# Kernel optimization log

Measured on AMD Instinct MI355X. Metric: run time of the kernel, lower is better.

## Reference

```python
import jax, jax.numpy as jnp
import numpy as np

B = 4096


def setup_inputs() -> dict:
    key = jax.random.key(0)
    u = jax.random.uniform(key, (B, 5), dtype=jnp.float32)
    centers = u[:, :2] * 64.0          # box centers in [0, 64)
    wh = u[:, 2:4] * 8.0 + 1.0         # widths/heights in [1, 9)
    ang = u[:, 4:5] * 3.14159265       # rotation angle in [0, pi)
    boxes = jnp.concatenate([centers, wh, ang], axis=-1)  # (B,5)
    return {"boxes": boxes}


def _rect_to_corners(boxes):
    # boxes: (B,5) = (x, y, w, h, theta) -> corners (B,4,2)
    unit = jnp.array([[-1.0, -1.0], [1.0, -1.0], [1.0, 1.0], [-1.0, 1.0]],
                     dtype=boxes.dtype)
    ctr, wh, ang = boxes[:, :2], boxes[:, 2:4], boxes[:, 4]
    base = unit[None, :, :] * (wh * 0.5)[:, None, :]        # (B,4,2)
    c, s = jnp.cos(ang), jnp.sin(ang)
    rot = jnp.stack([jnp.stack([c, -s], -1),
                     jnp.stack([s, c], -1)], axis=1)         # (B,2,2)
    return jnp.einsum('bkd,bde->bke', base, rot) + ctr[:, None, :]


def _giou1d(min1, max1, min2, max2):
    # exact (non-fast) 1-D GIoU per axis
    inter = jnp.clip(jnp.minimum(max1, max2) - jnp.maximum(min1, min2), 0.0)
    union = (max1 - min1) + (max2 - min2) - inter
    hull = jnp.maximum(max1, max2) - jnp.minimum(min1, min2)
    return inter / union - (hull - union) / hull


def reference(boxes):
    corners = _rect_to_corners(boxes)                        # (B,4,2)
    nb = corners.shape[0]
    # two edge axes per box: c1-c0 and c3-c0
    axes = jnp.stack([corners[:, 1] - corners[:, 0],
                      corners[:, 3] - corners[:, 0]], axis=1)  # (B,2,2)
    # self projections: box b's corners onto its own axes
    sp = jnp.einsum('bkd,bad->bak', corners, axes)           # (B,2,4)
    smin, smax = sp.min(-1), sp.max(-1)                      # (B,2)
    # cross projections: corners of box i onto axes of box j
    cp = jnp.einsum('ikd,jad->ijak', corners, axes)          # (B,B,2,4)
    cmin, cmax = cp.min(-1), cp.max(-1)                      # (B,B,2)
    # projections of box j's corners onto box i's axes = transpose of cross
    cminT, cmaxT = jnp.swapaxes(cmin, 0, 1), jnp.swapaxes(cmax, 0, 1)
    # axes of box i: (box i self) vs (box j projected on i's axes)
    gA = _giou1d(smin[:, None, :], smax[:, None, :], cminT, cmaxT)  # (B,B,2)
    # axes of box j: (box i projected on j's axes) vs (box j self)
    gB = _giou1d(cmin, cmax, smin[None, :, :], smax[None, :, :])    # (B,B,2)
    g = jnp.concatenate([gA, gB], axis=-1).min(-1)           # min over 4 axes
    pairwise = jnp.clip(g, 0.0)
    idx = jnp.arange(nb)
    pairwise = pairwise.at[idx, idx].set(0.0)                # zero diagonal
    return pairwise  # reduction='none' -> (B,B)
```

## Files before the change

### kernel.cpp

```cpp
#include <hip/hip_runtime.h>
#include <math.h>

#define NBOX 4096
#define TILE 32
#define NT (NBOX / TILE)
#define NTRI (NT * (NT + 1) / 2)
#define NBLK (NTRI / 4)
#define SS 12
#define JB 400
#define SLICE 800

typedef float v2f __attribute__((ext_vector_type(2)));
typedef float vf4 __attribute__((ext_vector_type(4)));


struct Box {
    v2f A0, A1, SC, LL;
    float cx, cy;
};

__device__ __forceinline__ float rcp_fast(float x) { return __builtin_amdgcn_rcpf(x); }
__device__ __forceinline__ v2f splat(float s) { return (v2f){s, s}; }
__device__ __forceinline__ v2f fma2(v2f a, v2f b, v2f c) { return __builtin_elementwise_fma(a, b, c); }
__device__ __forceinline__ v2f abs2(v2f a) { return __builtin_elementwise_abs(a); }
__device__ __forceinline__ v2f min2(v2f a, v2f b) { return __builtin_elementwise_min(a, b); }

__device__ __forceinline__ float mgiou_pair(const Box& I, const Box& J) {
    v2f dA = fma2(I.A0, splat(J.A0.x), I.A1 * J.A1.x);
    v2f dB = fma2(I.A0, splat(J.A0.y), I.A1 * J.A1.y);
    v2f DI = fma2(I.A0, splat(J.cx), fma2(I.A1, splat(J.cy), -I.SC));
    v2f DJ = fma2(J.A0, splat(I.cx), fma2(J.A1, splat(I.cy), -J.SC));
    v2f aA = abs2(dA), aB = abs2(dB);
    v2f HI = aA + aB;
    v2f HJ = (v2f){aA.x, aB.x} + (v2f){aA.y, aB.y};
    v2f SI = I.LL + HI;
    v2f SJ = J.LL + HJ;
    v2f uI = fma2(splat(0.5f), SI, -abs2(DI));
    v2f uJ = fma2(splat(0.5f), SJ, -abs2(DJ));
    v2f rI = min2(min2(I.LL, HI), uI);
    v2f rJ = min2(min2(J.LL, HJ), uJ);
    float S01 = SI.x * SI.y, S23 = SJ.x * SJ.y;
    float P = S01 * S23;
    v2f mI = rI * (v2f){SI.y, SI.x} * splat(S23);
    v2f mJ = rJ * (v2f){SJ.y, SJ.x} * splat(S01);
    float mm = fminf(fminf(mI.x, mI.y), fminf(mJ.x, mJ.y));
    return fmaxf(mm, 0.0f) * rcp_fast(P - mm);
}

__device__ __forceinline__ int sw_offset(int i) { return i * SS + (i >> 3) * 4; }

__device__ __forceinline__ Box load_box(const float* p) {
    Box b;
    float4 x = *(const float4*)(p);
    float4 y = *(const float4*)(p + 4);
    float2 z = *(const float2*)(p + 8);
    b.A0 = (v2f){x.x, x.y}; b.A1 = (v2f){x.z, x.w};
    b.SC = (v2f){y.x, y.y}; b.LL = (v2f){y.z, y.w};
    b.cx = z.x; b.cy = z.y;
    return b;
}

__device__ __forceinline__ void decode_tri(int k, int& bi, int& bj) {
    bi = (int)((float)(2 * NT + 1 - sqrtf((float)((2 * NT + 1) * (2 * NT + 1) - 8 * k))) * 0.5f);
    if (bi > 0 && k < bi * NT - bi * (bi - 1) / 2) bi--;
    if (k >= (bi + 1) * NT - (bi + 1) * bi / 2) bi++;
    bj = bi + (k - (bi * NT - bi * (bi - 1) / 2));
}

__global__ __launch_bounds__(256) __attribute__((amdgpu_waves_per_eu(4)))
void pairwise_kernel(const float* __restrict__ boxes, float* __restrict__ out) {
    __shared__ float sm[4 * SLICE];

    int tid = threadIdx.x;
    {
        int sid = tid >> 6, loc = tid & 63;
        int kP = 4 * blockIdx.x + sid;
        int biP, bjP; decode_tri(kP, biP, bjP);
        int box = ((loc < TILE) ? biP : bjP) * TILE + (loc & (TILE - 1));
        float cx = boxes[box * 5 + 0];
        float cy = boxes[box * 5 + 1];
        float w  = boxes[box * 5 + 2];
        float h  = boxes[box * 5 + 3];
        float ang = boxes[box * 5 + 4];
        float s, c;
        __sincosf(ang, &s, &c);
        float a0x = w * c, a0y = -w * s;
        float a1x = h * s, a1y =  h * c;
        float sc0 = fmaf(a0x, cx, a0y * cy);
        float sc1 = fmaf(a1x, cx, a1y * cy);
        float* d = &sm[sid * SLICE + ((loc < TILE) ? 0 : JB) + sw_offset(loc & (TILE - 1))];
        ((float4*)d)[0] = make_float4(a0x, a1x, a0y, a1y);
        ((float4*)d)[1] = make_float4(sc0, sc1, w * w, h * h);
        ((float2*)d)[4] = make_float2(cx, cy);
    }
    __syncthreads();

    int w = tid >> 6;
    int lane = tid & 63;
    int tx = lane & 7;
    int ty = lane >> 3;

    int k = 4 * blockIdx.x + w;
    int bi, bj; decode_tri(k, bi, bj);

    const float* base = &sm[w * SLICE];
    const float* ip = base + sw_offset(4 * ty);
    int ibase = bi * TILE, jbase = bj * TILE;
    bool offdiag = (bi != bj);

    #pragma unroll
    for (int c = 0; c < 2; ++c) {
        Box J0 = load_box(base + JB + sw_offset(4 * tx + 2 * c));
        Box J1 = load_box(base + JB + sw_offset(4 * tx + 2 * c + 1));
        int jg0 = jbase + 4 * tx + 2 * c;
        float vT0[4], vT1[4];
        #pragma unroll
        for (int kk = 0; kk < 4; ++kk) {
            Box I = load_box(ip + kk * SS);
            int ig = ibase + 4 * ty + kk;
            float v0 = (ig == jg0)     ? 0.0f : mgiou_pair(I, J0);
            float v1 = (ig == jg0 + 1) ? 0.0f : mgiou_pair(I, J1);
            vT0[kk] = v0; vT1[kk] = v1;
            v2f o = {v0, v1};
            *(v2f*)&out[(size_t)ig * NBOX + jg0] = o;
        }
        if (offdiag) {
            vf4 o0 = {vT0[0], vT0[1], vT0[2], vT0[3]};
            *(vf4*)&out[(size_t)jg0 * NBOX + ibase + 4 * ty] = o0;
            vf4 o1 = {vT1[0], vT1[1], vT1[2], vT1[3]};
            *(vf4*)&out[(size_t)(jg0 + 1) * NBOX + ibase + 4 * ty] = o1;
        }
    }
}

extern "C" void kernel_launch(void* const* d_in, const int* in_sizes, int n_in,
                              void* d_out, int out_size, void* d_ws, size_t ws_size,
                              hipStream_t stream) {
    const float* boxes = (const float*)d_in[0];
    float* out = (float*)d_out;
    pairwise_kernel<<<dim3(NBLK), dim3(256), 0, stream>>>(boxes, out);
}
```

Measured before the change: 81.44 us.

## Replace symmetric triangular tiling with row-strip blocks writing full rows

The kernel no longer computes only the upper-triangular tiles with mirrored transposed stores. Each block now owns 8 output rows and loops over 256-box column chunks staged in shared memory, computing every pair and writing contiguous float4 rows. This removes the scattered transposed writes and the triangular index decoding. In exchange it does roughly twice the pair arithmetic, recomputes the box transforms for every chunk in every block, and adds two block barriers per chunk.

```diff
diff --git a/kernel.cpp b/kernel.cpp
--- a/kernel.cpp
+++ b/kernel.cpp
@@ -2,13 +2,11 @@
 #include <math.h>
 
 #define NBOX 4096
-#define TILE 32
-#define NT (NBOX / TILE)
-#define NTRI (NT * (NT + 1) / 2)
-#define NBLK (NTRI / 4)
+#define ROWS 8
+#define CHUNK 256
+#define NCHUNK (NBOX / CHUNK)
+#define NBLK (NBOX / ROWS)
 #define SS 12
-#define JB 400
-#define SLICE 800
 
 typedef float v2f __attribute__((ext_vector_type(2)));
 typedef float vf4 __attribute__((ext_vector_type(4)));
@@ -60,76 +58,68 @@
     return b;
 }
 
-__device__ __forceinline__ void decode_tri(int k, int& bi, int& bj) {
-    bi = (int)((float)(2 * NT + 1 - sqrtf((float)((2 * NT + 1) * (2 * NT + 1) - 8 * k))) * 0.5f);
-    if (bi > 0 && k < bi * NT - bi * (bi - 1) / 2) bi--;
-    if (k >= (bi + 1) * NT - (bi + 1) * bi / 2) bi++;
-    bj = bi + (k - (bi * NT - bi * (bi - 1) / 2));
+__device__ __forceinline__ Box make_box(const float* __restrict__ boxes, int box) {
+    float cx = boxes[box * 5 + 0];
+    float cy = boxes[box * 5 + 1];
+    float w  = boxes[box * 5 + 2];
+    float h  = boxes[box * 5 + 3];
+    float ang = boxes[box * 5 + 4];
+    float s, c;
+    __sincosf(ang, &s, &c);
+    float a0x = w * c, a0y = -w * s;
+    float a1x = h * s, a1y =  h * c;
+    Box b;
+    b.A0 = (v2f){a0x, a1x};
+    b.A1 = (v2f){a0y, a1y};
+    b.SC = (v2f){fmaf(a0x, cx, a0y * cy), fmaf(a1x, cx, a1y * cy)};
+    b.LL = (v2f){w * w, h * h};
+    b.cx = cx; b.cy = cy;
+    return b;
 }
 
-__global__ __launch_bounds__(256) __attribute__((amdgpu_waves_per_eu(4)))
+__global__ __launch_bounds__(256)
 void pairwise_kernel(const float* __restrict__ boxes, float* __restrict__ out) {
-    __shared__ float sm[4 * SLICE];
+    __shared__ float sm[CHUNK * SS + (CHUNK / 8) * 4];
 
     int tid = threadIdx.x;
-    {
-        int sid = tid >> 6, loc = tid & 63;
-        int kP = 4 * blockIdx.x + sid;
-        int biP, bjP; decode_tri(kP, biP, bjP);
-        int box = ((loc < TILE) ? biP : bjP) * TILE + (loc & (TILE - 1));
-        float cx = boxes[box * 5 + 0];
-        float cy = boxes[box * 5 + 1];
-        float w  = boxes[box * 5 + 2];
-        float h  = boxes[box * 5 + 3];
-        float ang = boxes[box * 5 + 4];
-        float s, c;
-        __sincosf(ang, &s, &c);
-        float a0x = w * c, a0y = -w * s;
-        float a1x = h * s, a1y =  h * c;
-        float sc0 = fmaf(a0x, cx, a0y * cy);
-        float sc1 = fmaf(a1x, cx, a1y * cy);
-        float* d = &sm[sid * SLICE + ((loc < TILE) ? 0 : JB) + sw_offset(loc & (TILE - 1))];
-        ((float4*)d)[0] = make_float4(a0x, a1x, a0y, a1y);
-        ((float4*)d)[1] = make_float4(sc0, sc1, w * w, h * h);
-        ((float2*)d)[4] = make_float2(cx, cy);
-    }
-    __syncthreads();
+    int wave = tid >> 6;
+    int lane = tid & 63;
 
-    int w = tid >> 6;
-    int lane = tid & 63;
-    int tx = lane & 7;
-    int ty = lane >> 3;
+    int i0 = blockIdx.x * ROWS + 2 * wave;
+    Box I0 = make_box(boxes, i0);
+    Box I1 = make_box(boxes, i0 + 1);
 
-    int k = 4 * blockIdx.x + w;
-    int bi, bj; decode_tri(k, bi, bj);
+    for (int c = 0; c < NCHUNK; ++c) {
+        __syncthreads();
+        {
+            int box = c * CHUNK + tid;
+            Box b = make_box(boxes, box);
+            float* d = &sm[sw_offset(tid)];
+            ((float4*)d)[0] = make_float4(b.A0.x, b.A0.y, b.A1.x, b.A1.y);
+            ((float4*)d)[1] = make_float4(b.SC.x, b.SC.y, b.LL.x, b.LL.y);
+            ((float2*)d)[4] = make_float2(b.cx, b.cy);
+        }
+        __syncthreads();
 
-    const float* base = &sm[w * SLICE];
-    const float* ip = base + sw_offset(4 * ty);
-    int ibase = bi * TILE, jbase = bj * TILE;
-    bool offdiag = (bi != bj);
+        int jg0 = c * CHUNK + 4 * lane;
+        Box J0 = load_box(&sm[sw_offset(4 * lane + 0)]);
+        Box J1 = load_box(&sm[sw_offset(4 * lane + 1)]);
+        Box J2 = load_box(&sm[sw_offset(4 * lane + 2)]);
+        Box J3 = load_box(&sm[sw_offset(4 * lane + 3)]);
 
-    #pragma unroll
-    for (int c = 0; c < 2; ++c) {
-        Box J0 = load_box(base + JB + sw_offset(4 * tx + 2 * c));
-        Box J1 = load_box(base + JB + sw_offset(4 * tx + 2 * c + 1));
-        int jg0 = jbase + 4 * tx + 2 * c;
-        float vT0[4], vT1[4];
-        #pragma unroll
-        for (int kk = 0; kk < 4; ++kk) {
-            Box I = load_box(ip + kk * SS);
-            int ig = ibase + 4 * ty + kk;
-            float v0 = (ig == jg0)     ? 0.0f : mgiou_pair(I, J0);
-            float v1 = (ig == jg0 + 1) ? 0.0f : mgiou_pair(I, J1);
-            vT0[kk] = v0; vT1[kk] = v1;
-            v2f o = {v0, v1};
-            *(v2f*)&out[(size_t)ig * NBOX + jg0] = o;
-        }
-        if (offdiag) {
-            vf4 o0 = {vT0[0], vT0[1], vT0[2], vT0[3]};
-            *(vf4*)&out[(size_t)jg0 * NBOX + ibase + 4 * ty] = o0;
-            vf4 o1 = {vT1[0], vT1[1], vT1[2], vT1[3]};
-            *(vf4*)&out[(size_t)(jg0 + 1) * NBOX + ibase + 4 * ty] = o1;
-        }
+        float a0 = (i0     == jg0 + 0) ? 0.0f : mgiou_pair(I0, J0);
+        float a1 = (i0     == jg0 + 1) ? 0.0f : mgiou_pair(I0, J1);
+        float a2 = (i0     == jg0 + 2) ? 0.0f : mgiou_pair(I0, J2);
+        float a3 = (i0     == jg0 + 3) ? 0.0f : mgiou_pair(I0, J3);
+        vf4 oa = {a0, a1, a2, a3};
+        *(vf4*)&out[(size_t)i0 * NBOX + jg0] = oa;
+
+        float b0 = (i0 + 1 == jg0 + 0) ? 0.0f : mgiou_pair(I1, J0);
+        float b1 = (i0 + 1 == jg0 + 1) ? 0.0f : mgiou_pair(I1, J1);
+        float b2 = (i0 + 1 == jg0 + 2) ? 0.0f : mgiou_pair(I1, J2);
+        float b3 = (i0 + 1 == jg0 + 3) ? 0.0f : mgiou_pair(I1, J3);
+        vf4 ob = {b0, b1, b2, b3};
+        *(vf4*)&out[(size_t)(i0 + 1) * NBOX + jg0] = ob;
     }
 }
 
```

Result: slower. 97.46 us (+19.7%).
